# Optimization experiments

Hardware: AMD Instinct MI355X
Metric: run time of the kernel (lower is better)

Reference implementation:

```python
import jax, jax.numpy as jnp
import numpy as np

V, D, B, L = 100000, 64, 4096, 200

def setup_inputs() -> dict:
    key = jax.random.key(0)
    ks = jax.random.split(key, 10)
    s = 0.05  # keep activations in a sane range for sigmoid
    return {
        "item_ids": jax.random.randint(ks[0], (B,), 0, V),
        "history": jax.random.randint(ks[1], (B, L), 0, V),
        "hist_len": jax.random.randint(ks[2], (B,), 1, L + 1),
        "emb_table": jax.random.normal(ks[3], (V, D), jnp.float32) * s,
        "aW1": jax.random.normal(ks[4], (3 * D, D), jnp.float32) * s,
        "ab1": jnp.zeros((D,), jnp.float32),
        "aW2": jax.random.normal(ks[5], (D, 1), jnp.float32) * s,
        "ab2": jnp.zeros((1,), jnp.float32),
        "fW1": jax.random.normal(ks[6], (3 * D, 128), jnp.float32) * s,
        "fb1": jnp.zeros((128,), jnp.float32),
        "fW2": jax.random.normal(ks[7], (128, 64), jnp.float32) * s,
        "fb2": jnp.zeros((64,), jnp.float32),
        "fW3": jax.random.normal(ks[8], (64, 1), jnp.float32) * s,
        "fb3": jnp.zeros((1,), jnp.float32),
    }

def reference(item_ids, history, hist_len, emb_table, aW1, ab1, aW2, ab2,
              fW1, fb1, fW2, fb2, fW3, fb3):
    target = emb_table[item_ids]                      # [B, D]
    hist = emb_table[history]                         # [B, L, D]
    # original pads short histories with zero rows -> zero the padded tail
    mask = (jnp.arange(hist.shape[1])[None, :] < hist_len[:, None]).astype(hist.dtype)
    hist = hist * mask[..., None]
    tgt = jnp.broadcast_to(target[:, None, :], hist.shape)     # [B, L, D]
    # attention_fc takes 3*D features: (hist, target, hist*target)
    feat = jnp.concatenate([hist, tgt, hist * tgt], axis=-1)   # [B, L, 3D]
    h = jax.nn.relu(feat @ aW1 + ab1)                 # [B, L, D]
    scores = (h @ aW2 + ab2)[..., 0]                  # [B, L]
    # faithful to original: softmax over full padded length (no length mask)
    w = jax.nn.softmax(scores, axis=1)
    pooled = jnp.einsum('bl,bld->bd', w, hist)        # [B, D]
    comb = jnp.concatenate([target, pooled, pooled - target], axis=-1)  # [B, 3D]
    z = jax.nn.relu(comb @ fW1 + fb1)
    z = jax.nn.relu(z @ fW2 + fb2)
    return jax.nn.sigmoid(z @ fW3 + fb3)              # [B, 1]
```

## Files before the change

### kernel.cpp

```cpp
#include <hip/hip_runtime.h>
#include <hip/hip_bf16.h>

#define NV 100000
#define ND 64
#define NB 4096
#define NL 200
#define HST 72

typedef __bf16 bf16_t;
typedef __bf16 bf16x8 __attribute__((ext_vector_type(8)));
typedef float  f32x4  __attribute__((ext_vector_type(4)));

__global__ __launch_bounds__(256)
void din_cvt(const float* __restrict__ emb, bf16_t* __restrict__ embh)
{
    const long base = ((long)blockIdx.x * 256 + threadIdx.x) * 8;
    f32x4 a0 = *(const f32x4*)(emb + base);
    f32x4 a1 = *(const f32x4*)(emb + base + 4);
    bf16x8 o;
    #pragma unroll
    for (int i = 0; i < 4; ++i) { o[i] = (bf16_t)a0[i]; o[i + 4] = (bf16_t)a1[i]; }
    *(bf16x8*)(embh + base) = o;
}

template <bool BT>
__global__ __launch_bounds__(256, 5)
void din_kernel1(const int* __restrict__ item_ids,
                 const int* __restrict__ history,
                 const int* __restrict__ hist_len,
                 const float* __restrict__ emb,
                 const bf16_t* __restrict__ embh,
                 const float* __restrict__ aW1,
                 const float* __restrict__ ab1,
                 const float* __restrict__ aW2,
                 float* __restrict__ comb_ws)
{
    __shared__ __align__(16) bf16_t histA[208 * HST];
    __shared__ __align__(16) float sc_w[208];
    __shared__ float pp[256];
    __shared__ float tgt[64];
    __shared__ float cb[64];
    __shared__ float pooled[64];
    __shared__ float red[8];

    const int b    = blockIdx.x;
    const int tid  = threadIdx.x;
    const int item = item_ids[b];
    const int len  = hist_len[b];
    const int wave = tid >> 6, lane = tid & 63;
    const int col  = lane & 15, quad = lane >> 4;

    if (tid < 64) tgt[tid] = emb[(long)item * ND + tid];

    if constexpr (BT) {
        const int p  = tid & 1;
        const int lb = tid >> 1;
        const int l1 = 128 + lb;
        const int i0 = history[b * NL + (lb < NL ? lb : NL - 1)];
        const int i1 = history[b * NL + (l1 < NL ? l1 : NL - 1)];
        const bool v0 = lb < len, v1 = l1 < len;
        const bf16x8 z = (bf16x8)(bf16_t)0.f;
        bf16x8 r0[4] = {z, z, z, z}, r1[4] = {z, z, z, z};
        if (v0) {
            const bf16_t* s = embh + (long)i0 * ND + p * 32;
            #pragma unroll
            for (int j = 0; j < 4; ++j) r0[j] = *(const bf16x8*)(s + j * 8);
        }
        if (v1) {
            const bf16_t* s = embh + (long)i1 * ND + p * 32;
            #pragma unroll
            for (int j = 0; j < 4; ++j) r1[j] = *(const bf16x8*)(s + j * 8);
        }
        bf16_t* d0 = &histA[lb * HST + p * 32];
        #pragma unroll
        for (int j = 0; j < 4; ++j) *(bf16x8*)(d0 + j * 8) = r0[j];
        if (l1 < 208) {
            bf16_t* d1 = &histA[l1 * HST + p * 32];
            #pragma unroll
            for (int j = 0; j < 4; ++j) *(bf16x8*)(d1 + j * 8) = r1[j];
        }
    } else {
        const int p     = tid & 3;
        const int lbase = tid >> 2;
        int  idxs[4]; bool vs[4];
        #pragma unroll
        for (int pass = 0; pass < 4; ++pass) {
            int l  = pass * 64 + lbase;
            idxs[pass] = history[b * NL + (l < NL ? l : NL - 1)];
            vs[pass]   = l < len;
        }
        #pragma unroll
        for (int g = 0; g < 2; ++g) {
            f32x4 r[2][4];
            #pragma unroll
            for (int q = 0; q < 2; ++q) {
                int pass = g * 2 + q, l = pass * 64 + lbase;
                if (l < 208 && vs[pass]) {
                    const float* src = emb + (long)idxs[pass] * ND + p * 16;
                    #pragma unroll
                    for (int j = 0; j < 4; ++j) r[q][j] = *(const f32x4*)(src + j * 4);
                }
            }
            #pragma unroll
            for (int q = 0; q < 2; ++q) {
                int pass = g * 2 + q, l = pass * 64 + lbase;
                if (l < 208) {
                    bf16x8 o0 = (bf16x8)(bf16_t)0.f, o1 = (bf16x8)(bf16_t)0.f;
                    if (vs[pass]) {
                        #pragma unroll
                        for (int i = 0; i < 4; ++i) {
                            o0[i] = (bf16_t)r[q][0][i]; o0[i + 4] = (bf16_t)r[q][1][i];
                            o1[i] = (bf16_t)r[q][2][i]; o1[i + 4] = (bf16_t)r[q][3][i];
                        }
                    }
                    bf16_t* dst = &histA[l * HST + p * 16];
                    *(bf16x8*)(dst) = o0;
                    *(bf16x8*)(dst + 8) = o1;
                }
            }
        }
    }

    {
        const int n4 = (tid & 15) * 4;
        const int kp = tid >> 4;
        f32x4 t4  = *(const f32x4*)(emb + (long)item * ND + kp * 4);
        f32x4 wb0 = *(const f32x4*)(aW1 + (64 + kp * 4 + 0) * 64 + n4);
        f32x4 wb1 = *(const f32x4*)(aW1 + (64 + kp * 4 + 1) * 64 + n4);
        f32x4 wb2 = *(const f32x4*)(aW1 + (64 + kp * 4 + 2) * 64 + n4);
        f32x4 wb3 = *(const f32x4*)(aW1 + (64 + kp * 4 + 3) * 64 + n4);
        f32x4 c4;
        #pragma unroll
        for (int j = 0; j < 4; ++j)
            c4[j] = t4[0] * wb0[j] + t4[1] * wb1[j] + t4[2] * wb2[j] + t4[3] * wb3[j];
        #pragma unroll
        for (int j = 0; j < 4; ++j) {
            c4[j] += __shfl_xor(c4[j], 16, 64);
            c4[j] += __shfl_xor(c4[j], 32, 64);
        }
        if (lane < 16) *(f32x4*)&pp[wave * 64 + n4] = c4;
    }

    __syncthreads();

    if (tid < 64) cb[tid] = ab1[tid] + pp[tid] + pp[64 + tid] + pp[128 + tid] + pp[192 + tid];

    bf16x8 bfrag[4][2];
    #pragma unroll
    for (int kb = 0; kb < 2; ++kb) {
        f32x4 t0 = *(const f32x4*)&tgt[kb * 32 + quad * 8];
        f32x4 t1 = *(const f32x4*)&tgt[kb * 32 + quad * 8 + 4];
        #pragma unroll
        for (int nt = 0; nt < 4; ++nt) {
            const int n = nt * 16 + col;
            const float* pa = aW1 + (long)(kb * 32 + quad * 8) * 64 + n;
            const float* pc = pa + 128 * 64;
            float wa[8], wc[8];
            #pragma unroll
            for (int j = 0; j < 8; ++j) { wa[j] = pa[j * 64]; wc[j] = pc[j * 64]; }
            bf16x8 w;
            #pragma unroll
            for (int j = 0; j < 8; ++j) {
                float tk = (j < 4) ? t0[j] : t1[j - 4];
                w[j] = (bf16_t)(wa[j] + tk * wc[j]);
            }
            bfrag[nt][kb] = w;
        }
    }
    float a2vals[4];
    #pragma unroll
    for (int nt = 0; nt < 4; ++nt) a2vals[nt] = aW2[nt * 16 + col];

    __syncthreads();
    float cvals[4];
    #pragma unroll
    for (int nt = 0; nt < 4; ++nt) cvals[nt] = cb[nt * 16 + col];

    for (int mt = wave; mt < 13; mt += 4) {
        const bf16_t* arow = &histA[(mt * 16 + col) * HST + quad * 8];
        bf16x8 af0 = *(const bf16x8*)(arow);
        bf16x8 af1 = *(const bf16x8*)(arow + 32);
        float sc[4] = {0.f, 0.f, 0.f, 0.f};
        #pragma unroll
        for (int nt = 0; nt < 4; ++nt) {
            f32x4 acc = {0.f, 0.f, 0.f, 0.f};
            acc = __builtin_amdgcn_mfma_f32_16x16x32_bf16(af0, bfrag[nt][0], acc, 0, 0, 0);
            acc = __builtin_amdgcn_mfma_f32_16x16x32_bf16(af1, bfrag[nt][1], acc, 0, 0, 0);
            #pragma unroll
            for (int i = 0; i < 4; ++i) {
                float h = acc[i] + cvals[nt];
                h = h > 0.f ? h : 0.f;
                sc[i] += h * a2vals[nt];
            }
        }
        #pragma unroll
        for (int off = 1; off < 16; off <<= 1)
            #pragma unroll
            for (int i = 0; i < 4; ++i) sc[i] += __shfl_xor(sc[i], off, 64);
        if (col == 0) {
            f32x4 outv = {sc[0], sc[1], sc[2], sc[3]};
            *(f32x4*)&sc_w[mt * 16 + quad * 4] = outv;
        }
    }
    __syncthreads();

    {
        float s = (tid < NL) ? sc_w[tid] : -1e30f;
        float m = s;
        #pragma unroll
        for (int off = 32; off > 0; off >>= 1) m = fmaxf(m, __shfl_xor(m, off, 64));
        if (lane == 0) red[wave] = m;
        __syncthreads();
        m = fmaxf(fmaxf(red[0], red[1]), fmaxf(red[2], red[3]));
        float e = (tid < NL) ? __expf(s - m) : 0.f;
        float ssum = e;
        #pragma unroll
        for (int off = 32; off > 0; off >>= 1) ssum += __shfl_xor(ssum, off, 64);
        if (lane == 0) red[4 + wave] = ssum;
        __syncthreads();
        float tot = red[4] + red[5] + red[6] + red[7];
        if (tid < NL) sc_w[tid] = e / tot;
    }
    __syncthreads();

    {
        float acc = 0.f;
        for (int l = wave; l < NL; l += 4)
            acc += sc_w[l] * (float)histA[l * HST + lane];
        pp[wave * 64 + lane] = acc;
    }
    __syncthreads();
    if (tid < 64) pooled[tid] = pp[tid] + pp[64 + tid] + pp[128 + tid] + pp[192 + tid];
    __syncthreads();

    if (tid < 192) {
        float v;
        if (tid < 64)       v = tgt[tid];
        else if (tid < 128) v = pooled[tid - 64];
        else                v = pooled[tid - 128] - tgt[tid - 128];
        comb_ws[(long)b * 192 + tid] = v;
    }
}

__global__ __launch_bounds__(256)
void din_kernel2(const float* __restrict__ comb,
                 const float* __restrict__ fW1, const float* __restrict__ fb1,
                 const float* __restrict__ fW2, const float* __restrict__ fb2,
                 const float* __restrict__ fW3, const float* __restrict__ fb3,
                 float* __restrict__ out)
{
    __shared__ float combs[4 * 192];
    __shared__ float z1s[4 * 128];
    const int tid = threadIdx.x;
    const int rb  = blockIdx.x * 4;

    for (int i = tid; i < 4 * 192; i += 256) combs[i] = comb[(long)rb * 192 + i];
    __syncthreads();

    {
        const int j  = tid & 127;
        const int r0 = (tid >> 7) * 2, r1 = r0 + 1;
        float a0 = fb1[j], a1 = a0;
        #pragma unroll 4
        for (int i = 0; i < 192; ++i) {
            float w = fW1[i * 128 + j];
            a0 += combs[r0 * 192 + i] * w;
            a1 += combs[r1 * 192 + i] * w;
        }
        z1s[r0 * 128 + j] = fmaxf(a0, 0.f);
        z1s[r1 * 128 + j] = fmaxf(a1, 0.f);
    }
    __syncthreads();

    {
        const int j2 = tid & 63;
        const int r2 = tid >> 6;
        float acc = fb2[j2];
        #pragma unroll 4
        for (int i = 0; i < 128; ++i)
            acc += z1s[r2 * 128 + i] * fW2[i * 64 + j2];
        float s = fmaxf(acc, 0.f) * fW3[j2];
        #pragma unroll
        for (int off = 1; off < 64; off <<= 1) s += __shfl_xor(s, off, 64);
        if (j2 == 0) out[rb + r2] = 1.f / (1.f + __expf(-(s + fb3[0])));
    }
}

extern "C" void kernel_launch(void* const* d_in, const int* in_sizes, int n_in,
                              void* d_out, int out_size, void* d_ws, size_t ws_size,
                              hipStream_t stream) {
    const int*   item_ids = (const int*)d_in[0];
    const int*   history  = (const int*)d_in[1];
    const int*   hist_len = (const int*)d_in[2];
    const float* emb      = (const float*)d_in[3];
    const float* aW1      = (const float*)d_in[4];
    const float* ab1      = (const float*)d_in[5];
    const float* aW2      = (const float*)d_in[6];
    const float* fW1      = (const float*)d_in[8];
    const float* fb1      = (const float*)d_in[9];
    const float* fW2      = (const float*)d_in[10];
    const float* fb2      = (const float*)d_in[11];
    const float* fW3      = (const float*)d_in[12];
    const float* fb3      = (const float*)d_in[13];

    const size_t embh_bytes = (size_t)NV * ND * sizeof(bf16_t);
    const size_t comb_bytes = (size_t)NB * 192 * sizeof(float);
    const bool   use_bt     = ws_size >= embh_bytes + comb_bytes;

    if (use_bt) {
        bf16_t* embh = (bf16_t*)d_ws;
        float*  comb = (float*)((char*)d_ws + embh_bytes);
        din_cvt<<<(NV * ND) / (256 * 8), 256, 0, stream>>>(emb, embh);
        din_kernel1<true><<<NB, 256, 0, stream>>>(item_ids, history, hist_len, emb,
                                                  embh, aW1, ab1, aW2, comb);
        din_kernel2<<<NB / 4, 256, 0, stream>>>(comb, fW1, fb1, fW2, fb2, fW3, fb3,
                                                (float*)d_out);
    } else {
        float* comb = (float*)d_ws;
        din_kernel1<false><<<NB, 256, 0, stream>>>(item_ids, history, hist_len, emb,
                                                   (const bf16_t*)nullptr, aW1, ab1, aW2, comb);
        din_kernel2<<<NB / 4, 256, 0, stream>>>(comb, fW1, fb1, fW2, fb2, fW3, fb3,
                                                (float*)d_out);
    }
}
```

Before: 169.6 us.

## Process one batch row per wave with register-streamed online softmax pooling

Each wave now handles a whole batch row instead of a 256-thread block per row. History rows are gathered straight into MFMA A-fragments in registers with one-tile-ahead prefetch, and the shared-memory staging is removed. Softmax and weighted pooling are fused into a single pass using a running max and rescaled accumulators, which drops all __syncthreads and LDS traffic. The cost is higher register pressure (launch bounds lowered to 4) and more per-wave serial work across 13 tiles, with fewer blocks in flight.

```diff
diff --git a/kernel.cpp b/kernel.cpp
--- a/kernel.cpp
+++ b/kernel.cpp
@@ -5,7 +5,6 @@
 #define ND 64
 #define NB 4096
 #define NL 200
-#define HST 72
 
 typedef __bf16 bf16_t;
 typedef __bf16 bf16x8 __attribute__((ext_vector_type(8)));
@@ -24,7 +23,7 @@
 }
 
 template <bool BT>
-__global__ __launch_bounds__(256, 5)
+__global__ __launch_bounds__(256, 4)
 void din_kernel1(const int* __restrict__ item_ids,
                  const int* __restrict__ history,
                  const int* __restrict__ hist_len,
@@ -35,134 +34,69 @@
                  const float* __restrict__ aW2,
                  float* __restrict__ comb_ws)
 {
-    __shared__ __align__(16) bf16_t histA[208 * HST];
-    __shared__ __align__(16) float sc_w[208];
-    __shared__ float pp[256];
-    __shared__ float tgt[64];
-    __shared__ float cb[64];
-    __shared__ float pooled[64];
-    __shared__ float red[8];
-
-    const int b    = blockIdx.x;
     const int tid  = threadIdx.x;
+    const int wave = tid >> 6, lane = tid & 63;
+    const int b    = blockIdx.x * 4 + wave;
+    const int col  = lane & 15, quad = lane >> 4;
+
     const int item = item_ids[b];
     const int len  = hist_len[b];
-    const int wave = tid >> 6, lane = tid & 63;
-    const int col  = lane & 15, quad = lane >> 4;
-
-    if (tid < 64) tgt[tid] = emb[(long)item * ND + tid];
-
-    if constexpr (BT) {
-        const int p  = tid & 1;
-        const int lb = tid >> 1;
-        const int l1 = 128 + lb;
-        const int i0 = history[b * NL + (lb < NL ? lb : NL - 1)];
-        const int i1 = history[b * NL + (l1 < NL ? l1 : NL - 1)];
-        const bool v0 = lb < len, v1 = l1 < len;
-        const bf16x8 z = (bf16x8)(bf16_t)0.f;
-        bf16x8 r0[4] = {z, z, z, z}, r1[4] = {z, z, z, z};
-        if (v0) {
-            const bf16_t* s = embh + (long)i0 * ND + p * 32;
-            #pragma unroll
-            for (int j = 0; j < 4; ++j) r0[j] = *(const bf16x8*)(s + j * 8);
-        }
-        if (v1) {
-            const bf16_t* s = embh + (long)i1 * ND + p * 32;
-            #pragma unroll
-            for (int j = 0; j < 4; ++j) r1[j] = *(const bf16x8*)(s + j * 8);
-        }
-        bf16_t* d0 = &histA[lb * HST + p * 32];
-        #pragma unroll
-        for (int j = 0; j < 4; ++j) *(bf16x8*)(d0 + j * 8) = r0[j];
-        if (l1 < 208) {
-            bf16_t* d1 = &histA[l1 * HST + p * 32];
-            #pragma unroll
-            for (int j = 0; j < 4; ++j) *(bf16x8*)(d1 + j * 8) = r1[j];
-        }
-    } else {
-        const int p     = tid & 3;
-        const int lbase = tid >> 2;
-        int  idxs[4]; bool vs[4];
-        #pragma unroll
-        for (int pass = 0; pass < 4; ++pass) {
-            int l  = pass * 64 + lbase;
-            idxs[pass] = history[b * NL + (l < NL ? l : NL - 1)];
-            vs[pass]   = l < len;
-        }
-        #pragma unroll
-        for (int g = 0; g < 2; ++g) {
-            f32x4 r[2][4];
-            #pragma unroll
-            for (int q = 0; q < 2; ++q) {
-                int pass = g * 2 + q, l = pass * 64 + lbase;
-                if (l < 208 && vs[pass]) {
-                    const float* src = emb + (long)idxs[pass] * ND + p * 16;
-                    #pragma unroll
-                    for (int j = 0; j < 4; ++j) r[q][j] = *(const f32x4*)(src + j * 4);
-                }
+    const float* trow = emb + (long)item * ND;
+
+    int idxs[13];
+    #pragma unroll
+    for (int mt = 0; mt < 13; ++mt) {
+        int l = mt * 16 + col;
+        idxs[mt] = history[b * NL + (l < NL ? l : NL - 1)];
+    }
+
+    f32x4 tA0a = *(const f32x4*)(trow + quad * 8);
+    f32x4 tA0b = *(const f32x4*)(trow + quad * 8 + 4);
+    f32x4 tA1a = *(const f32x4*)(trow + 32 + quad * 8);
+    f32x4 tA1b = *(const f32x4*)(trow + 32 + quad * 8 + 4);
+    f32x4 tc0  = *(const f32x4*)(trow + quad * 16);
+    f32x4 tc1  = *(const f32x4*)(trow + quad * 16 + 4);
+    f32x4 tc2  = *(const f32x4*)(trow + quad * 16 + 8);
+    f32x4 tc3  = *(const f32x4*)(trow + quad * 16 + 12);
+
+    float cvals[4];
+    {
+        float part[4];
+        #pragma unroll
+        for (int nt = 0; nt < 4; ++nt) {
+            const int n = nt * 16 + col;
+            const float* pb = aW1 + (long)(64 + quad * 16) * 64 + n;
+            float s = 0.f;
+            #pragma unroll
+            for (int j = 0; j < 16; ++j) {
+                float tk = (j < 4) ? tc0[j] : (j < 8) ? tc1[j - 4]
+                         : (j < 12) ? tc2[j - 8] : tc3[j - 12];
+                s += tk * pb[j * 64];
             }
-            #pragma unroll
-            for (int q = 0; q < 2; ++q) {
-                int pass = g * 2 + q, l = pass * 64 + lbase;
-                if (l < 208) {
-                    bf16x8 o0 = (bf16x8)(bf16_t)0.f, o1 = (bf16x8)(bf16_t)0.f;
-                    if (vs[pass]) {
-                        #pragma unroll
-                        for (int i = 0; i < 4; ++i) {
-                            o0[i] = (bf16_t)r[q][0][i]; o0[i + 4] = (bf16_t)r[q][1][i];
-                            o1[i] = (bf16_t)r[q][2][i]; o1[i + 4] = (bf16_t)r[q][3][i];
-                        }
-                    }
-                    bf16_t* dst = &histA[l * HST + p * 16];
-                    *(bf16x8*)(dst) = o0;
-                    *(bf16x8*)(dst + 8) = o1;
-                }
-            }
-        }
-    }
-
-    {
-        const int n4 = (tid & 15) * 4;
-        const int kp = tid >> 4;
-        f32x4 t4  = *(const f32x4*)(emb + (long)item * ND + kp * 4);
-        f32x4 wb0 = *(const f32x4*)(aW1 + (64 + kp * 4 + 0) * 64 + n4);
-        f32x4 wb1 = *(const f32x4*)(aW1 + (64 + kp * 4 + 1) * 64 + n4);
-        f32x4 wb2 = *(const f32x4*)(aW1 + (64 + kp * 4 + 2) * 64 + n4);
-        f32x4 wb3 = *(const f32x4*)(aW1 + (64 + kp * 4 + 3) * 64 + n4);
-        f32x4 c4;
-        #pragma unroll
-        for (int j = 0; j < 4; ++j)
-            c4[j] = t4[0] * wb0[j] + t4[1] * wb1[j] + t4[2] * wb2[j] + t4[3] * wb3[j];
-        #pragma unroll
-        for (int j = 0; j < 4; ++j) {
-            c4[j] += __shfl_xor(c4[j], 16, 64);
-            c4[j] += __shfl_xor(c4[j], 32, 64);
-        }
-        if (lane < 16) *(f32x4*)&pp[wave * 64 + n4] = c4;
-    }
-
-    __syncthreads();
-
-    if (tid < 64) cb[tid] = ab1[tid] + pp[tid] + pp[64 + tid] + pp[128 + tid] + pp[192 + tid];
+            part[nt] = s;
+        }
+        #pragma unroll
+        for (int nt = 0; nt < 4; ++nt) {
+            part[nt] += __shfl_xor(part[nt], 16, 64);
+            part[nt] += __shfl_xor(part[nt], 32, 64);
+            cvals[nt] = part[nt] + ab1[nt * 16 + col];
+        }
+    }
 
     bf16x8 bfrag[4][2];
     #pragma unroll
     for (int kb = 0; kb < 2; ++kb) {
-        f32x4 t0 = *(const f32x4*)&tgt[kb * 32 + quad * 8];
-        f32x4 t1 = *(const f32x4*)&tgt[kb * 32 + quad * 8 + 4];
         #pragma unroll
         for (int nt = 0; nt < 4; ++nt) {
             const int n = nt * 16 + col;
             const float* pa = aW1 + (long)(kb * 32 + quad * 8) * 64 + n;
             const float* pc = pa + 128 * 64;
-            float wa[8], wc[8];
-            #pragma unroll
-            for (int j = 0; j < 8; ++j) { wa[j] = pa[j * 64]; wc[j] = pc[j * 64]; }
             bf16x8 w;
             #pragma unroll
             for (int j = 0; j < 8; ++j) {
-                float tk = (j < 4) ? t0[j] : t1[j - 4];
-                w[j] = (bf16_t)(wa[j] + tk * wc[j]);
+                float tk = (kb == 0) ? ((j < 4) ? tA0a[j] : tA0b[j - 4])
+                                     : ((j < 4) ? tA1a[j] : tA1b[j - 4]);
+                w[j] = (bf16_t)(pa[j * 64] + tk * pc[j * 64]);
             }
             bfrag[nt][kb] = w;
         }
@@ -171,15 +105,39 @@
     #pragma unroll
     for (int nt = 0; nt < 4; ++nt) a2vals[nt] = aW2[nt * 16 + col];
 
-    __syncthreads();
-    float cvals[4];
-    #pragma unroll
-    for (int nt = 0; nt < 4; ++nt) cvals[nt] = cb[nt * 16 + col];
-
-    for (int mt = wave; mt < 13; mt += 4) {
-        const bf16_t* arow = &histA[(mt * 16 + col) * HST + quad * 8];
-        bf16x8 af0 = *(const bf16x8*)(arow);
-        bf16x8 af1 = *(const bf16x8*)(arow + 32);
+    auto load_rows = [&](int mt, bf16x8& o0, bf16x8& o1) {
+        if constexpr (BT) {
+            const bf16_t* s = embh + (long)idxs[mt] * ND + quad * 8;
+            o0 = *(const bf16x8*)(s);
+            o1 = *(const bf16x8*)(s + 32);
+        } else {
+            const float* s = emb + (long)idxs[mt] * ND + quad * 8;
+            f32x4 a0 = *(const f32x4*)(s),      a1 = *(const f32x4*)(s + 4);
+            f32x4 a2 = *(const f32x4*)(s + 32), a3 = *(const f32x4*)(s + 36);
+            #pragma unroll
+            for (int i = 0; i < 4; ++i) {
+                o0[i] = (bf16_t)a0[i]; o0[i + 4] = (bf16_t)a1[i];
+                o1[i] = (bf16_t)a2[i]; o1[i + 4] = (bf16_t)a3[i];
+            }
+        }
+    };
+
+    float mrun = -1e30f, Z = 0.f;
+    float po0[8], po1[8];
+    #pragma unroll
+    for (int j = 0; j < 8; ++j) { po0[j] = 0.f; po1[j] = 0.f; }
+
+    bf16x8 naf0, naf1;
+    load_rows(0, naf0, naf1);
+
+    #pragma unroll
+    for (int mt = 0; mt < 13; ++mt) {
+        bf16x8 af0 = naf0, af1 = naf1;
+        if (mt + 1 < 13) load_rows(mt + 1, naf0, naf1);
+
+        const bool valid = (mt * 16 + col) < len;
+        if (!valid) { af0 = (bf16x8)(bf16_t)0.f; af1 = (bf16x8)(bf16_t)0.f; }
+
         float sc[4] = {0.f, 0.f, 0.f, 0.f};
         #pragma unroll
         for (int nt = 0; nt < 4; ++nt) {
@@ -197,48 +155,72 @@
         for (int off = 1; off < 16; off <<= 1)
             #pragma unroll
             for (int i = 0; i < 4; ++i) sc[i] += __shfl_xor(sc[i], off, 64);
-        if (col == 0) {
-            f32x4 outv = {sc[0], sc[1], sc[2], sc[3]};
-            *(f32x4*)&sc_w[mt * 16 + quad * 4] = outv;
-        }
-    }
-    __syncthreads();
-
-    {
-        float s = (tid < NL) ? sc_w[tid] : -1e30f;
-        float m = s;
-        #pragma unroll
-        for (int off = 32; off > 0; off >>= 1) m = fmaxf(m, __shfl_xor(m, off, 64));
-        if (lane == 0) red[wave] = m;
-        __syncthreads();
-        m = fmaxf(fmaxf(red[0], red[1]), fmaxf(red[2], red[3]));
-        float e = (tid < NL) ? __expf(s - m) : 0.f;
-        float ssum = e;
-        #pragma unroll
-        for (int off = 32; off > 0; off >>= 1) ssum += __shfl_xor(ssum, off, 64);
-        if (lane == 0) red[4 + wave] = ssum;
-        __syncthreads();
-        float tot = red[4] + red[5] + red[6] + red[7];
-        if (tid < NL) sc_w[tid] = e / tot;
-    }
-    __syncthreads();
-
-    {
-        float acc = 0.f;
-        for (int l = wave; l < NL; l += 4)
-            acc += sc_w[l] * (float)histA[l * HST + lane];
-        pp[wave * 64 + lane] = acc;
-    }
-    __syncthreads();
-    if (tid < 64) pooled[tid] = pp[tid] + pp[64 + tid] + pp[128 + tid] + pp[192 + tid];
-    __syncthreads();
-
-    if (tid < 192) {
-        float v;
-        if (tid < 64)       v = tgt[tid];
-        else if (tid < 128) v = pooled[tid - 64];
-        else                v = pooled[tid - 128] - tgt[tid - 128];
-        comb_ws[(long)b * 192 + tid] = v;
+
+        #pragma unroll
+        for (int i = 0; i < 4; ++i)
+            if (mt * 16 + quad * 4 + i >= NL) sc[i] = -1e30f;
+
+        float tm = fmaxf(fmaxf(sc[0], sc[1]), fmaxf(sc[2], sc[3]));
+        tm = fmaxf(tm, __shfl_xor(tm, 16, 64));
+        tm = fmaxf(tm, __shfl_xor(tm, 32, 64));
+        float mnew  = fmaxf(mrun, tm);
+        float alpha = __expf(mrun - mnew);
+
+        float e[4];
+        #pragma unroll
+        for (int i = 0; i < 4; ++i) e[i] = __expf(sc[i] - mnew);
+        float zt = e[0] + e[1] + e[2] + e[3];
+        zt += __shfl_xor(zt, 16, 64);
+        zt += __shfl_xor(zt, 32, 64);
+        Z = Z * alpha + zt;
+        mrun = mnew;
+
+        float esel = (col & 2) ? ((col & 1) ? e[3] : e[2])
+                               : ((col & 1) ? e[1] : e[0]);
+        float p = __shfl(esel, (col >> 2) * 16 + col, 64);
+
+        #pragma unroll
+        for (int j = 0; j < 8; ++j) {
+            po0[j] = po0[j] * alpha + p * (float)af0[j];
+            po1[j] = po1[j] * alpha + p * (float)af1[j];
+        }
+    }
+
+    #pragma unroll
+    for (int off = 1; off < 16; off <<= 1)
+        #pragma unroll
+        for (int j = 0; j < 8; ++j) {
+            po0[j] += __shfl_xor(po0[j], off, 64);
+            po1[j] += __shfl_xor(po1[j], off, 64);
+        }
+    const float invZ = 1.f / Z;
+    #pragma unroll
+    for (int j = 0; j < 8; ++j) { po0[j] *= invZ; po1[j] *= invZ; }
+
+    float* cw = comb_ws + (long)b * 192;
+    if (col == 2) {
+        *(f32x4*)(cw + quad * 8)          = tA0a;
+        *(f32x4*)(cw + quad * 8 + 4)      = tA0b;
+        *(f32x4*)(cw + 32 + quad * 8)     = tA1a;
+        *(f32x4*)(cw + 32 + quad * 8 + 4) = tA1b;
+    } else if (col == 0) {
+        f32x4 v0 = {po0[0], po0[1], po0[2], po0[3]};
+        f32x4 v1 = {po0[4], po0[5], po0[6], po0[7]};
+        f32x4 v2 = {po1[0], po1[1], po1[2], po1[3]};
+        f32x4 v3 = {po1[4], po1[5], po1[6], po1[7]};
+        *(f32x4*)(cw + 64 + quad * 8)          = v0;
+        *(f32x4*)(cw + 64 + quad * 8 + 4)      = v1;
+        *(f32x4*)(cw + 96 + quad * 8)          = v2;
+        *(f32x4*)(cw + 96 + quad * 8 + 4)      = v3;
+    } else if (col == 1) {
+        f32x4 v0 = {po0[0] - tA0a[0], po0[1] - tA0a[1], po0[2] - tA0a[2], po0[3] - tA0a[3]};
+        f32x4 v1 = {po0[4] - tA0b[0], po0[5] - tA0b[1], po0[6] - tA0b[2], po0[7] - tA0b[3]};
+        f32x4 v2 = {po1[0] - tA1a[0], po1[1] - tA1a[1], po1[2] - tA1a[2], po1[3] - tA1a[3]};
+        f32x4 v3 = {po1[4] - tA1b[0], po1[5] - tA1b[1], po1[6] - tA1b[2], po1[7] - tA1b[3]};
+        *(f32x4*)(cw + 128 + quad * 8)          = v0;
+        *(f32x4*)(cw + 128 + quad * 8 + 4)      = v1;
+        *(f32x4*)(cw + 160 + quad * 8)          = v2;
+        *(f32x4*)(cw + 160 + quad * 8 + 4)      = v3;
     }
 }
 
@@ -311,14 +293,14 @@
         bf16_t* embh = (bf16_t*)d_ws;
         float*  comb = (float*)((char*)d_ws + embh_bytes);
         din_cvt<<<(NV * ND) / (256 * 8), 256, 0, stream>>>(emb, embh);
-        din_kernel1<true><<<NB, 256, 0, stream>>>(item_ids, history, hist_len, emb,
-                                                  embh, aW1, ab1, aW2, comb);
+        din_kernel1<true><<<NB / 4, 256, 0, stream>>>(item_ids, history, hist_len, emb,
+                                                      embh, aW1, ab1, aW2, comb);
         din_kernel2<<<NB / 4, 256, 0, stream>>>(comb, fW1, fb1, fW2, fb2, fW3, fb3,
                                                 (float*)d_out);
     } else {
         float* comb = (float*)d_ws;
-        din_kernel1<false><<<NB, 256, 0, stream>>>(item_ids, history, hist_len, emb,
-                                                   (const bf16_t*)nullptr, aW1, ab1, aW2, comb);
+        din_kernel1<false><<<NB / 4, 256, 0, stream>>>(item_ids, history, hist_len, emb,
+                                                       (const bf16_t*)nullptr, aW1, ab1, aW2, comb);
         din_kernel2<<<NB / 4, 256, 0, stream>>>(comb, fW1, fb1, fW2, fb2, fW3, fb3,
                                                 (float*)d_out);
     }
```

After: 438.8 us. 2.59x slower.

## Swizzle LDS history layout and stage folded attention weights through shared memory

Applied to the files above, without the earlier changes.

Replaces the padded row stride of the history tile with an XOR-swizzled 64-wide layout, and rewrites the gather so each thread loads one 16-byte segment per row across more passes. The folded first-layer weight (Wa + t*Wc) is now computed once per block into a swizzled shared-memory transposed tile, and MFMA B fragments are read from there instead of each lane issuing strided global loads. The constant term is computed in the same pass. This adds 8KB of LDS and lowers the occupancy hint from 5 to 4 blocks per CU, trading occupancy for fewer redundant global weight reads and bank-conflict-free fragment loads.

```diff
diff --git a/kernel.cpp b/kernel.cpp
--- a/kernel.cpp
+++ b/kernel.cpp
@@ -5,10 +5,10 @@
 #define ND 64
 #define NB 4096
 #define NL 200
-#define HST 72
 
 typedef __bf16 bf16_t;
 typedef __bf16 bf16x8 __attribute__((ext_vector_type(8)));
+typedef __bf16 bf16x4 __attribute__((ext_vector_type(4)));
 typedef float  f32x4  __attribute__((ext_vector_type(4)));
 
 __global__ __launch_bounds__(256)
@@ -24,7 +24,7 @@
 }
 
 template <bool BT>
-__global__ __launch_bounds__(256, 5)
+__global__ __launch_bounds__(256, 4)
 void din_kernel1(const int* __restrict__ item_ids,
                  const int* __restrict__ history,
                  const int* __restrict__ hist_len,
@@ -35,7 +35,8 @@
                  const float* __restrict__ aW2,
                  float* __restrict__ comb_ws)
 {
-    __shared__ __align__(16) bf16_t histA[208 * HST];
+    __shared__ __align__(16) bf16_t histA[208 * 64];
+    __shared__ __align__(16) bf16_t wbT[64 * 64];
     __shared__ __align__(16) float sc_w[208];
     __shared__ float pp[256];
     __shared__ float tgt[64];
@@ -49,96 +50,68 @@
     const int len  = hist_len[b];
     const int wave = tid >> 6, lane = tid & 63;
     const int col  = lane & 15, quad = lane >> 4;
+    const int c7   = col & 7;
 
     if (tid < 64) tgt[tid] = emb[(long)item * ND + tid];
 
     if constexpr (BT) {
-        const int p  = tid & 1;
-        const int lb = tid >> 1;
-        const int l1 = 128 + lb;
-        const int i0 = history[b * NL + (lb < NL ? lb : NL - 1)];
-        const int i1 = history[b * NL + (l1 < NL ? l1 : NL - 1)];
-        const bool v0 = lb < len, v1 = l1 < len;
-        const bf16x8 z = (bf16x8)(bf16_t)0.f;
-        bf16x8 r0[4] = {z, z, z, z}, r1[4] = {z, z, z, z};
-        if (v0) {
-            const bf16_t* s = embh + (long)i0 * ND + p * 32;
-            #pragma unroll
-            for (int j = 0; j < 4; ++j) r0[j] = *(const bf16x8*)(s + j * 8);
-        }
-        if (v1) {
-            const bf16_t* s = embh + (long)i1 * ND + p * 32;
-            #pragma unroll
-            for (int j = 0; j < 4; ++j) r1[j] = *(const bf16x8*)(s + j * 8);
-        }
-        bf16_t* d0 = &histA[lb * HST + p * 32];
-        #pragma unroll
-        for (int j = 0; j < 4; ++j) *(bf16x8*)(d0 + j * 8) = r0[j];
-        if (l1 < 208) {
-            bf16_t* d1 = &histA[l1 * HST + p * 32];
-            #pragma unroll
-            for (int j = 0; j < 4; ++j) *(bf16x8*)(d1 + j * 8) = r1[j];
+        const int seg = tid & 7;
+        const int rl  = tid >> 3;
+        #pragma unroll
+        for (int pass = 0; pass < 7; ++pass) {
+            const int l = pass * 32 + rl;
+            if (l < 208) {
+                const int lc  = l < NL ? l : NL - 1;
+                const int idx = history[b * NL + lc];
+                bf16x8 v = (bf16x8)(bf16_t)0.f;
+                if (l < len) v = *(const bf16x8*)(embh + (long)idx * ND + seg * 8);
+                *(bf16x8*)&histA[l * 64 + ((seg ^ (l & 7)) * 8)] = v;
+            }
         }
     } else {
-        const int p     = tid & 3;
-        const int lbase = tid >> 2;
-        int  idxs[4]; bool vs[4];
-        #pragma unroll
-        for (int pass = 0; pass < 4; ++pass) {
-            int l  = pass * 64 + lbase;
-            idxs[pass] = history[b * NL + (l < NL ? l : NL - 1)];
-            vs[pass]   = l < len;
-        }
-        #pragma unroll
-        for (int g = 0; g < 2; ++g) {
-            f32x4 r[2][4];
-            #pragma unroll
-            for (int q = 0; q < 2; ++q) {
-                int pass = g * 2 + q, l = pass * 64 + lbase;
-                if (l < 208 && vs[pass]) {
-                    const float* src = emb + (long)idxs[pass] * ND + p * 16;
+        const int seg = tid & 15;
+        const int rl  = tid >> 4;
+        #pragma unroll
+        for (int pass = 0; pass < 13; ++pass) {
+            const int l = pass * 16 + rl;
+            if (l < 208) {
+                const int lc  = l < NL ? l : NL - 1;
+                const int idx = history[b * NL + lc];
+                bf16x4 v = (bf16x4)(bf16_t)0.f;
+                if (l < len) {
+                    f32x4 a = *(const f32x4*)(emb + (long)idx * ND + seg * 4);
                     #pragma unroll
-                    for (int j = 0; j < 4; ++j) r[q][j] = *(const f32x4*)(src + j * 4);
+                    for (int i = 0; i < 4; ++i) v[i] = (bf16_t)a[i];
                 }
+                *(bf16x4*)&histA[l * 64 + (((seg >> 1) ^ (l & 7)) * 8) + (seg & 1) * 4] = v;
             }
-            #pragma unroll
-            for (int q = 0; q < 2; ++q) {
-                int pass = g * 2 + q, l = pass * 64 + lbase;
-                if (l < 208) {
-                    bf16x8 o0 = (bf16x8)(bf16_t)0.f, o1 = (bf16x8)(bf16_t)0.f;
-                    if (vs[pass]) {
-                        #pragma unroll
-                        for (int i = 0; i < 4; ++i) {
-                            o0[i] = (bf16_t)r[q][0][i]; o0[i + 4] = (bf16_t)r[q][1][i];
-                            o1[i] = (bf16_t)r[q][2][i]; o1[i + 4] = (bf16_t)r[q][3][i];
-                        }
-                    }
-                    bf16_t* dst = &histA[l * HST + p * 16];
-                    *(bf16x8*)(dst) = o0;
-                    *(bf16x8*)(dst + 8) = o1;
-                }
-            }
-        }
-    }
-
-    {
-        const int n4 = (tid & 15) * 4;
-        const int kp = tid >> 4;
-        f32x4 t4  = *(const f32x4*)(emb + (long)item * ND + kp * 4);
-        f32x4 wb0 = *(const f32x4*)(aW1 + (64 + kp * 4 + 0) * 64 + n4);
-        f32x4 wb1 = *(const f32x4*)(aW1 + (64 + kp * 4 + 1) * 64 + n4);
-        f32x4 wb2 = *(const f32x4*)(aW1 + (64 + kp * 4 + 2) * 64 + n4);
-        f32x4 wb3 = *(const f32x4*)(aW1 + (64 + kp * 4 + 3) * 64 + n4);
-        f32x4 c4;
-        #pragma unroll
-        for (int j = 0; j < 4; ++j)
-            c4[j] = t4[0] * wb0[j] + t4[1] * wb1[j] + t4[2] * wb2[j] + t4[3] * wb3[j];
-        #pragma unroll
-        for (int j = 0; j < 4; ++j) {
-            c4[j] += __shfl_xor(c4[j], 16, 64);
-            c4[j] += __shfl_xor(c4[j], 32, 64);
-        }
-        if (lane < 16) *(f32x4*)&pp[wave * 64 + n4] = c4;
+        }
+    }
+
+    {
+        const int n  = tid & 63;
+        const int kp = tid >> 6;
+        const float* tq = emb + (long)item * ND + kp * 16;
+        f32x4 t0 = *(const f32x4*)(tq);
+        f32x4 t1 = *(const f32x4*)(tq + 4);
+        f32x4 t2 = *(const f32x4*)(tq + 8);
+        f32x4 t3 = *(const f32x4*)(tq + 12);
+        float tk[16];
+        #pragma unroll
+        for (int i = 0; i < 4; ++i) {
+            tk[i] = t0[i]; tk[4 + i] = t1[i]; tk[8 + i] = t2[i]; tk[12 + i] = t3[i];
+        }
+        float csum = 0.f;
+        #pragma unroll
+        for (int i = 0; i < 16; ++i) {
+            const int k = kp * 16 + i;
+            float wa = aW1[k * 64 + n];
+            float wc = aW1[(128 + k) * 64 + n];
+            float wb = aW1[(64 + k) * 64 + n];
+            wbT[n * 64 + (((k >> 3) ^ (n & 7)) * 8) + (k & 7)] = (bf16_t)(wa + tk[i] * wc);
+            csum += tk[i] * wb;
+        }
+        pp[tid] = csum;
     }
 
     __syncthreads();
@@ -147,26 +120,10 @@
 
     bf16x8 bfrag[4][2];
     #pragma unroll
-    for (int kb = 0; kb < 2; ++kb) {
-        f32x4 t0 = *(const f32x4*)&tgt[kb * 32 + quad * 8];
-        f32x4 t1 = *(const f32x4*)&tgt[kb * 32 + quad * 8 + 4];
-        #pragma unroll
-        for (int nt = 0; nt < 4; ++nt) {
-            const int n = nt * 16 + col;
-            const float* pa = aW1 + (long)(kb * 32 + quad * 8) * 64 + n;
-            const float* pc = pa + 128 * 64;
-            float wa[8], wc[8];
-            #pragma unroll
-            for (int j = 0; j < 8; ++j) { wa[j] = pa[j * 64]; wc[j] = pc[j * 64]; }
-            bf16x8 w;
-            #pragma unroll
-            for (int j = 0; j < 8; ++j) {
-                float tk = (j < 4) ? t0[j] : t1[j - 4];
-                w[j] = (bf16_t)(wa[j] + tk * wc[j]);
-            }
-            bfrag[nt][kb] = w;
-        }
-    }
+    for (int nt = 0; nt < 4; ++nt)
+        #pragma unroll
+        for (int kb = 0; kb < 2; ++kb)
+            bfrag[nt][kb] = *(const bf16x8*)&wbT[(nt * 16 + col) * 64 + (((kb * 4 + quad) ^ c7) * 8)];
     float a2vals[4];
     #pragma unroll
     for (int nt = 0; nt < 4; ++nt) a2vals[nt] = aW2[nt * 16 + col];
@@ -177,9 +134,9 @@
     for (int nt = 0; nt < 4; ++nt) cvals[nt] = cb[nt * 16 + col];
 
     for (int mt = wave; mt < 13; mt += 4) {
-        const bf16_t* arow = &histA[(mt * 16 + col) * HST + quad * 8];
-        bf16x8 af0 = *(const bf16x8*)(arow);
-        bf16x8 af1 = *(const bf16x8*)(arow + 32);
+        const bf16_t* arow = &histA[(mt * 16 + col) * 64];
+        bf16x8 af0 = *(const bf16x8*)(arow + ((quad ^ c7) * 8));
+        bf16x8 af1 = *(const bf16x8*)(arow + (((4 + quad) ^ c7) * 8));
         float sc[4] = {0.f, 0.f, 0.f, 0.f};
         #pragma unroll
         for (int nt = 0; nt < 4; ++nt) {
@@ -225,8 +182,10 @@
 
     {
         float acc = 0.f;
-        for (int l = wave; l < NL; l += 4)
-            acc += sc_w[l] * (float)histA[l * HST + lane];
+        for (int l = wave; l < NL; l += 4) {
+            const int pos = l * 64 + (((lane >> 3) ^ (l & 7)) * 8) + (lane & 7);
+            acc += sc_w[l] * (float)histA[pos];
+        }
         pp[wave * 64 + lane] = acc;
     }
     __syncthreads();
```

Result: no change. 170.4 us (+0.5%).
